# Optimization experiments

Measured on AMD Instinct MI355X. Metric: run time of the kernel, lower is better.

The kernel has to match this reference:

```python
import jax, jax.numpy as jnp
import numpy as np

N = 4096
TAU = 0.2          # args.tau relaxation temperature
EPS = 1e-10        # numerical guard for logit of clamped probs


def setup_inputs() -> dict:
    key = jax.random.key(0)
    k1, k2, k3 = jax.random.split(key, 3)
    r = jax.random.uniform(k1, (N, N))
    ori_adj = jnp.where(r < 0.005, -1.0, jnp.where(r < 0.01, 1.0, 0.0)).astype(jnp.float32)
    # nn.init.uniform_(change_links_prob, 0.0, 0.001)
    change_links_prob = jax.random.uniform(k2, (N, N), minval=0.0, maxval=0.001, dtype=jnp.float32)
    # uniform noise for the RelaxedBernoulli logistic reparameterization
    u = jax.random.uniform(k3, (N, N), minval=1e-6, maxval=1.0 - 1e-6, dtype=jnp.float32)
    return {"ori_adj": ori_adj, "change_links_prob": change_links_prob, "u": u}


def reference(ori_adj, change_links_prob, u):
    # --- get_modified_adj: RelaxedBernoulliStraightThrough(tau, clamp(p,0,1)).rsample() ---
    p = jnp.clip(change_links_prob, EPS, 1.0 - EPS)      # torch.clamp(p, 0, 1) + logit guard
    logits = jnp.log(p) - jnp.log1p(-p)
    noise = jnp.log(u) - jnp.log1p(-u)                   # logistic noise
    soft = jax.nn.sigmoid((logits + noise) / TAU)        # relaxed sample
    hard = jnp.round(soft)                               # quantized sample
    change_prob = soft + jax.lax.stop_gradient(hard - soft)  # straight-through
    mod_adj = ori_adj + change_prob * (-2.0 * ori_adj)   # ori_adj * (1 - 2*b)

    # --- balance_degree_directed(mod_adj) ---
    # torch.diag(matrix) returns the diagonal VECTOR, broadcast-subtracted per row (faithful).
    A = mod_adj + mod_adj.T - jnp.diag(mod_adj)
    A_abs = jnp.abs(A)
    tr3 = jnp.einsum('ij,jk,ki->', A, A, A)              # trace(A @ A @ A)
    tr3_abs = jnp.einsum('ij,jk,ki->', A_abs, A_abs, A_abs)
    balance = 0.5 * (1.0 + tr3 / tr3_abs)
    return mod_adj, balance
```

## Files before the change

kernel.cpp:

```cpp
#include <hip/hip_runtime.h>
#include <hip/hip_bf16.h>
#include <cstdint>
#include <cstddef>

#define N 4096
#define NN ((size_t)N * (size_t)N)

typedef int int4v __attribute__((ext_vector_type(4)));

__device__ inline void async16(const void* g, void* lds) {
    __builtin_amdgcn_global_load_lds(
        (const __attribute__((address_space(1))) void*)g,
        (__attribute__((address_space(3))) void*)lds, 16, 0, 0);
}

__global__ void mod_kernel(const float* __restrict__ ori,
                           const float* __restrict__ clp,
                           const float* __restrict__ u,
                           float* __restrict__ out) {
    size_t i = (size_t)blockIdx.x * blockDim.x + threadIdx.x;
    if (i >= NN) return;
    float p = clp[i];
    p = fminf(fmaxf(p, 1e-10f), 1.0f - 1e-10f);
    float logits = logf(p) - log1pf(-p);
    float uu = u[i];
    float noise = logf(uu) - log1pf(-uu);
    float y = (logits + noise) / 0.2f;
    float soft = 1.0f / (1.0f + expf(-y));
    float hard = rintf(soft);
    float o = ori[i];
    out[i] = o + hard * (-2.0f * o);
}

__global__ void diag_kernel(const float* __restrict__ mod,
                            float* __restrict__ diag,
                            double* __restrict__ accs) {
    int j = blockIdx.x * blockDim.x + threadIdx.x;
    if (j < N) diag[j] = mod[(size_t)j * N + j];
    if (blockIdx.x == 0 && threadIdx.x < 2) accs[threadIdx.x] = 0.0;
}

__global__ void build_A8(const float* __restrict__ mod,
                         const float* __restrict__ diag,
                         signed char* __restrict__ A,
                         signed char* __restrict__ AT,
                         signed char* __restrict__ Aa,
                         signed char* __restrict__ ATa) {
    __shared__ float tji[32][33];
    __shared__ signed char cv[32][36];
    const int bi = blockIdx.x * 32;
    const int bj = blockIdx.y * 32;
    const int tx = threadIdx.x;
    const int ty = threadIdx.y;
    {
        const float4 v = *(const float4*)&mod[(size_t)(bj + ty) * N + bi + tx * 4];
        tji[ty][tx * 4 + 0] = v.x; tji[ty][tx * 4 + 1] = v.y;
        tji[ty][tx * 4 + 2] = v.z; tji[ty][tx * 4 + 3] = v.w;
    }
    __syncthreads();
    const float4 mv = *(const float4*)&mod[(size_t)(bi + ty) * N + bj + tx * 4];
    float m4[4] = {mv.x, mv.y, mv.z, mv.w};
    int pkA = 0, pkAa = 0;
    #pragma unroll
    for (int k = 0; k < 4; ++k) {
        int jl = tx * 4 + k;
        float a = m4[k] + tji[jl][ty] - diag[bj + jl];
        int ai = (int)a;
        cv[ty][jl] = (signed char)ai;
        int au = ai < 0 ? -ai : ai;
        pkA  |= (ai & 255) << (8 * k);
        pkAa |= (au & 255) << (8 * k);
    }
    *(int*)&A [(size_t)(bi + ty) * N + bj + tx * 4] = pkA;
    *(int*)&Aa[(size_t)(bi + ty) * N + bj + tx * 4] = pkAa;
    __syncthreads();
    int pkT = 0, pkTa = 0;
    #pragma unroll
    for (int k = 0; k < 4; ++k) {
        int il = tx * 4 + k;
        int v = cv[il][ty];
        int va = v < 0 ? -v : v;
        pkT  |= (v  & 255) << (8 * k);
        pkTa |= (va & 255) << (8 * k);
    }
    *(int*)&AT [(size_t)(bj + ty) * N + bi + tx * 4] = pkT;
    *(int*)&ATa[(size_t)(bj + ty) * N + bi + tx * 4] = pkTa;
}

__global__ __launch_bounds__(256) void gemm_trace_i8(const signed char* __restrict__ Ag,
                                                     const signed char* __restrict__ ATg,
                                                     const signed char* __restrict__ Aag,
                                                     const signed char* __restrict__ ATag,
                                                     double* __restrict__ accs) {
    __shared__ int4v As4[512];
    __shared__ int4v Bs4[512];
    __shared__ int red[4];
    const int z = blockIdx.z;
    const signed char* Asrc = z ? Aag  : Ag;
    const signed char* Bsrc = z ? ATag : ATg;
    const int i0 = blockIdx.y * 128;
    const int k0 = blockIdx.x * 128;
    const int t = threadIdx.x;
    const int lane = t & 63;
    const int wave = t >> 6;
    const int quad = lane >> 4;
    const int col  = lane & 15;
    const int wr = (wave >> 1) * 64;
    const int wc = (wave & 1) * 64;
    signed char* Asc = (signed char*)As4;
    signed char* Bsc = (signed char*)Bs4;

    const int c0 = wave * 64 + lane;
    const int c1 = c0 + 256;
    const int r0 = c0 >> 2, r1 = c1 >> 2;
    const int cc0 = (((c0 & 3) ^ ((r0 >> 1) & 3)) << 4);
    const int cc1 = (((c1 & 3) ^ ((r1 >> 1) & 3)) << 4);
    const int ldsb0 = (wave * 64) << 4;
    const int ldsb1 = (256 + wave * 64) << 4;
    const signed char* gA0 = Asrc + (size_t)(i0 + r0) * N + cc0;
    const signed char* gA1 = Asrc + (size_t)(i0 + r1) * N + cc1;
    const signed char* gB0 = Bsrc + (size_t)(k0 + r0) * N + cc0;
    const signed char* gB1 = Bsrc + (size_t)(k0 + r1) * N + cc1;

    int4v acc[4][4];
    #pragma unroll
    for (int a = 0; a < 4; ++a)
        #pragma unroll
        for (int b = 0; b < 4; ++b)
            acc[a][b] = (int4v){0, 0, 0, 0};

    const int fsw = ((quad ^ ((col >> 1) & 3)) << 4);

    for (int kb = 0; kb < N; kb += 64) {
        __syncthreads();
        async16(gA0 + kb, Asc + ldsb0);
        async16(gA1 + kb, Asc + ldsb1);
        async16(gB0 + kb, Bsc + ldsb0);
        async16(gB1 + kb, Bsc + ldsb1);
        __syncthreads();
        int4v af[4], bf[4];
        #pragma unroll
        for (int tr = 0; tr < 4; ++tr)
            af[tr] = *(const int4v*)(Asc + ((wr + tr * 16 + col) << 6) + fsw);
        #pragma unroll
        for (int tc = 0; tc < 4; ++tc)
            bf[tc] = *(const int4v*)(Bsc + ((wc + tc * 16 + col) << 6) + fsw);
        #pragma unroll
        for (int tr = 0; tr < 4; ++tr)
            #pragma unroll
            for (int tc = 0; tc < 4; ++tc)
                acc[tr][tc] = __builtin_amdgcn_mfma_i32_16x16x64_i8(af[tr], bf[tc], acc[tr][tc], 0, 0, 0);
    }

    int part = 0;
    #pragma unroll
    for (int tr = 0; tr < 4; ++tr) {
        #pragma unroll
        for (int tc = 0; tc < 4; ++tc) {
            const int ib = i0 + wr + tr * 16 + quad * 4;
            const int kk = k0 + wc + tc * 16 + col;
            #pragma unroll
            for (int r = 0; r < 4; ++r)
                part += acc[tr][tc][r] * (int)Bsrc[(size_t)(ib + r) * N + kk];
        }
    }
    #pragma unroll
    for (int off = 32; off > 0; off >>= 1)
        part += __shfl_down(part, off, 64);
    if (lane == 0) red[wave] = part;
    __syncthreads();
    if (t == 0) {
        int tot = red[0] + red[1] + red[2] + red[3];
        atomicAdd(&accs[z], (double)tot);
    }
}

__global__ void finalize_kernel(const double* __restrict__ accs, float* __restrict__ out) {
    out[NN] = (float)(0.5 * (1.0 + accs[0] / accs[1]));
}

extern "C" void kernel_launch(void* const* d_in, const int* in_sizes, int n_in,
                              void* d_out, int out_size, void* d_ws, size_t ws_size,
                              hipStream_t stream) {
    const float* ori = (const float*)d_in[0];
    const float* clp = (const float*)d_in[1];
    const float* u   = (const float*)d_in[2];
    float* out = (float*)d_out;
    char* ws = (char*)d_ws;
    signed char* A8   = (signed char*)ws;
    signed char* AT8  = (signed char*)(ws + NN);
    signed char* Aa8  = (signed char*)(ws + 2 * NN);
    signed char* ATa8 = (signed char*)(ws + 3 * NN);
    float*       diag = (float*)(ws + 4 * NN);
    double*      accs = (double*)(ws + 4 * NN + 4096 * 4);

    mod_kernel<<<dim3((unsigned)(NN / 256)), 256, 0, stream>>>(ori, clp, u, out);
    diag_kernel<<<dim3(16), 256, 0, stream>>>(out, diag, accs);
    build_A8<<<dim3(N / 32, N / 32), dim3(8, 32), 0, stream>>>(out, diag, A8, AT8, Aa8, ATa8);
    gemm_trace_i8<<<dim3(N / 128, N / 128, 2), 256, 0, stream>>>(A8, AT8, Aa8, ATa8, accs);
    finalize_kernel<<<1, 1, 0, stream>>>(accs, out);
}
```

Measured before the change: 427.0 us.

## Deepen GEMM K-step to 128, vectorize mod kernel, fold diag into build

The int8 trace GEMM now stages 128 K-columns per iteration, doubling the LDS tiles and halving the number of barrier pairs per K sweep. The elementwise mod kernel is vectorized to float4 per thread and also zeroes the accumulators. The separate diag kernel is removed; build_A8 loads the needed diagonal entries into shared memory itself. The aim is fewer launches and less synchronization overhead, at the cost of more LDS per block, which may reduce occupancy.

After: 435.0 us. About the same (+1.9%).

```diff
diff --git a/kernel.cpp b/kernel.cpp
--- a/kernel.cpp
+++ b/kernel.cpp
@@ -14,39 +14,40 @@
         (__attribute__((address_space(3))) void*)lds, 16, 0, 0);
 }
 
-__global__ void mod_kernel(const float* __restrict__ ori,
-                           const float* __restrict__ clp,
-                           const float* __restrict__ u,
-                           float* __restrict__ out) {
+__global__ void mod_kernel(const float4* __restrict__ ori,
+                           const float4* __restrict__ clp,
+                           const float4* __restrict__ u,
+                           float4* __restrict__ out,
+                           double* __restrict__ accs) {
     size_t i = (size_t)blockIdx.x * blockDim.x + threadIdx.x;
-    if (i >= NN) return;
-    float p = clp[i];
-    p = fminf(fmaxf(p, 1e-10f), 1.0f - 1e-10f);
-    float logits = logf(p) - log1pf(-p);
-    float uu = u[i];
-    float noise = logf(uu) - log1pf(-uu);
-    float y = (logits + noise) / 0.2f;
-    float soft = 1.0f / (1.0f + expf(-y));
-    float hard = rintf(soft);
-    float o = ori[i];
-    out[i] = o + hard * (-2.0f * o);
-}
-
-__global__ void diag_kernel(const float* __restrict__ mod,
-                            float* __restrict__ diag,
-                            double* __restrict__ accs) {
-    int j = blockIdx.x * blockDim.x + threadIdx.x;
-    if (j < N) diag[j] = mod[(size_t)j * N + j];
+    float4 o4 = ori[i], p4 = clp[i], u4 = u[i];
+    float po[4] = {p4.x, p4.y, p4.z, p4.w};
+    float uo[4] = {u4.x, u4.y, u4.z, u4.w};
+    float oo[4] = {o4.x, o4.y, o4.z, o4.w};
+    float ro[4];
+    #pragma unroll
+    for (int k = 0; k < 4; ++k) {
+        float p = fminf(fmaxf(po[k], 1e-10f), 1.0f - 1e-10f);
+        float logits = logf(p) - log1pf(-p);
+        float uu = uo[k];
+        float noise = logf(uu) - log1pf(-uu);
+        float y = (logits + noise) / 0.2f;
+        float soft = 1.0f / (1.0f + expf(-y));
+        float hard = rintf(soft);
+        float o = oo[k];
+        ro[k] = o + hard * (-2.0f * o);
+    }
+    out[i] = make_float4(ro[0], ro[1], ro[2], ro[3]);
     if (blockIdx.x == 0 && threadIdx.x < 2) accs[threadIdx.x] = 0.0;
 }
 
 __global__ void build_A8(const float* __restrict__ mod,
-                         const float* __restrict__ diag,
                          signed char* __restrict__ A,
                          signed char* __restrict__ AT,
                          signed char* __restrict__ Aa,
                          signed char* __restrict__ ATa) {
     __shared__ float tji[32][33];
+    __shared__ float dloc[32];
     __shared__ signed char cv[32][36];
     const int bi = blockIdx.x * 32;
     const int bj = blockIdx.y * 32;
@@ -57,6 +58,7 @@
         tji[ty][tx * 4 + 0] = v.x; tji[ty][tx * 4 + 1] = v.y;
         tji[ty][tx * 4 + 2] = v.z; tji[ty][tx * 4 + 3] = v.w;
     }
+    if (tx == 0) dloc[ty] = mod[(size_t)(bj + ty) * N + bj + ty];
     __syncthreads();
     const float4 mv = *(const float4*)&mod[(size_t)(bi + ty) * N + bj + tx * 4];
     float m4[4] = {mv.x, mv.y, mv.z, mv.w};
@@ -64,7 +66,7 @@
     #pragma unroll
     for (int k = 0; k < 4; ++k) {
         int jl = tx * 4 + k;
-        float a = m4[k] + tji[jl][ty] - diag[bj + jl];
+        float a = m4[k] + tji[jl][ty] - dloc[jl];
         int ai = (int)a;
         cv[ty][jl] = (signed char)ai;
         int au = ai < 0 ? -ai : ai;
@@ -92,8 +94,8 @@
                                                      const signed char* __restrict__ Aag,
                                                      const signed char* __restrict__ ATag,
                                                      double* __restrict__ accs) {
-    __shared__ int4v As4[512];
-    __shared__ int4v Bs4[512];
+    __shared__ int4v As4[1024];
+    __shared__ int4v Bs4[1024];
     __shared__ int red[4];
     const int z = blockIdx.z;
     const signed char* Asrc = z ? Aag  : Ag;
@@ -110,17 +112,12 @@
     signed char* Asc = (signed char*)As4;
     signed char* Bsc = (signed char*)Bs4;
 
-    const int c0 = wave * 64 + lane;
-    const int c1 = c0 + 256;
-    const int r0 = c0 >> 2, r1 = c1 >> 2;
-    const int cc0 = (((c0 & 3) ^ ((r0 >> 1) & 3)) << 4);
-    const int cc1 = (((c1 & 3) ^ ((r1 >> 1) & 3)) << 4);
-    const int ldsb0 = (wave * 64) << 4;
-    const int ldsb1 = (256 + wave * 64) << 4;
-    const signed char* gA0 = Asrc + (size_t)(i0 + r0) * N + cc0;
-    const signed char* gA1 = Asrc + (size_t)(i0 + r1) * N + cc1;
-    const signed char* gB0 = Bsrc + (size_t)(k0 + r0) * N + cc0;
-    const signed char* gB1 = Bsrc + (size_t)(k0 + r1) * N + cc1;
+    const int r0 = t >> 2;
+    const int s0 = t & 3;
+    const int c0 = s0 ^ ((r0 >> 1) & 3);
+    const signed char* gA = Asrc + (size_t)(i0 + r0) * N + c0 * 16;
+    const signed char* gB = Bsrc + (size_t)(k0 + r0) * N + c0 * 16;
+    const int ldst = t * 16;
 
     int4v acc[4][4];
     #pragma unroll
@@ -131,25 +128,42 @@
 
     const int fsw = ((quad ^ ((col >> 1) & 3)) << 4);
 
-    for (int kb = 0; kb < N; kb += 64) {
+    for (int kb = 0; kb < N; kb += 128) {
         __syncthreads();
-        async16(gA0 + kb, Asc + ldsb0);
-        async16(gA1 + kb, Asc + ldsb1);
-        async16(gB0 + kb, Bsc + ldsb0);
-        async16(gB1 + kb, Bsc + ldsb1);
+        const signed char* ga = gA + kb;
+        const signed char* gb = gB + kb;
+        async16(ga,              Asc + ldst);
+        async16(ga + 64 * N,     Asc + 4096  + ldst);
+        async16(ga + 64,         Asc + 8192  + ldst);
+        async16(ga + 64 * N + 64, Asc + 12288 + ldst);
+        async16(gb,              Bsc + ldst);
+        async16(gb + 64 * N,     Bsc + 4096  + ldst);
+        async16(gb + 64,         Bsc + 8192  + ldst);
+        async16(gb + 64 * N + 64, Bsc + 12288 + ldst);
         __syncthreads();
-        int4v af[4], bf[4];
-        #pragma unroll
-        for (int tr = 0; tr < 4; ++tr)
-            af[tr] = *(const int4v*)(Asc + ((wr + tr * 16 + col) << 6) + fsw);
-        #pragma unroll
-        for (int tc = 0; tc < 4; ++tc)
-            bf[tc] = *(const int4v*)(Bsc + ((wc + tc * 16 + col) << 6) + fsw);
+        int4v af0[4], af1[4], bf0[4], bf1[4];
+        #pragma unroll
+        for (int tr = 0; tr < 4; ++tr) {
+            const int ra = (wr + tr * 16 + col) << 6;
+            af0[tr] = *(const int4v*)(Asc + ra + fsw);
+            af1[tr] = *(const int4v*)(Asc + 8192 + ra + fsw);
+        }
+        #pragma unroll
+        for (int tc = 0; tc < 4; ++tc) {
+            const int rb = (wc + tc * 16 + col) << 6;
+            bf0[tc] = *(const int4v*)(Bsc + rb + fsw);
+            bf1[tc] = *(const int4v*)(Bsc + 8192 + rb + fsw);
+        }
         #pragma unroll
         for (int tr = 0; tr < 4; ++tr)
             #pragma unroll
             for (int tc = 0; tc < 4; ++tc)
-                acc[tr][tc] = __builtin_amdgcn_mfma_i32_16x16x64_i8(af[tr], bf[tc], acc[tr][tc], 0, 0, 0);
+                acc[tr][tc] = __builtin_amdgcn_mfma_i32_16x16x64_i8(af0[tr], bf0[tc], acc[tr][tc], 0, 0, 0);
+        #pragma unroll
+        for (int tr = 0; tr < 4; ++tr)
+            #pragma unroll
+            for (int tc = 0; tc < 4; ++tc)
+                acc[tr][tc] = __builtin_amdgcn_mfma_i32_16x16x64_i8(af1[tr], bf1[tc], acc[tr][tc], 0, 0, 0);
     }
 
     int part = 0;
@@ -191,12 +205,11 @@
     signed char* AT8  = (signed char*)(ws + NN);
     signed char* Aa8  = (signed char*)(ws + 2 * NN);
     signed char* ATa8 = (signed char*)(ws + 3 * NN);
-    float*       diag = (float*)(ws + 4 * NN);
-    double*      accs = (double*)(ws + 4 * NN + 4096 * 4);
-
-    mod_kernel<<<dim3((unsigned)(NN / 256)), 256, 0, stream>>>(ori, clp, u, out);
-    diag_kernel<<<dim3(16), 256, 0, stream>>>(out, diag, accs);
-    build_A8<<<dim3(N / 32, N / 32), dim3(8, 32), 0, stream>>>(out, diag, A8, AT8, Aa8, ATa8);
+    double*      accs = (double*)(ws + 4 * NN);
+
+    mod_kernel<<<dim3((unsigned)(NN / 1024)), 256, 0, stream>>>(
+        (const float4*)ori, (const float4*)clp, (const float4*)u, (float4*)out, accs);
+    build_A8<<<dim3(N / 32, N / 32), dim3(8, 32), 0, stream>>>(out, A8, AT8, Aa8, ATa8);
     gemm_trace_i8<<<dim3(N / 128, N / 128, 2), 256, 0, stream>>>(A8, AT8, Aa8, ATa8, accs);
     finalize_kernel<<<1, 1, 0, stream>>>(accs, out);
 }
```
